# Kernel tuning notes

Hardware: AMD Instinct MI355X
Metric: run time of the kernel (lower is better)

## Reference

```python
import jax, jax.numpy as jnp
import numpy as np

KD, KY, KX = 3, 3, 3  # kernel_size from init_kwargs


def setup_inputs() -> dict:
    key = jax.random.key(0)
    x = jax.random.normal(key, (4, 2, 64, 256, 256), dtype=jnp.float32)
    return {"x": x}


def reference(x):
    # x: [B, CH, D, H, W]
    B, CH, D, H, W = x.shape
    pd, py, px = (KD - 1) // 2, (KY - 1) // 2, (KX - 1) // 2
    # replicate padding (torch F.pad mode='replicate' == jnp.pad mode='edge')
    xp = jnp.pad(x, ((0, 0), (0, 0), (pd, pd), (py, py), (px, px)), mode='edge')
    center = (KD * KY * KX) // 2  # flattened center position, excluded from max
    # running max over the 26 non-center neighbors; never materializes the
    # [B, CH, 27, D, H, W] tensor the torch conv3d path creates.
    max_nc = jnp.full(x.shape, -jnp.inf, dtype=x.dtype)
    idx = 0
    for i in range(KD):
        for j in range(KY):
            for k in range(KX):
                if idx != center:
                    shifted = xp[:, :, i:i + D, j:j + H, k:k + W]
                    max_nc = jnp.maximum(max_nc, shifted)
                idx += 1
    mask = x > max_nc  # strict local maximum (excluding self)
    return x * mask.astype(x.dtype)
```

## Files before the change

kernel.cpp:

```cpp
#include <hip/hip_runtime.h>


constexpr int D_   = 64;
constexpr int H_   = 256;
constexpr int W_   = 256;
constexpr int HW_  = H_ * W_;
constexpr int NVOL = 8;
constexpr int DC   = 8;

__device__ __forceinline__ float f3(float a, float b, float c) {
    return fmaxf(fmaxf(a, b), c);
}

__global__ __launch_bounds__(256, 4)
void nms3d(const float* __restrict__ x, float* __restrict__ out)
{
    const int tx = threadIdx.x;
    const int ty = threadIdx.y;
    const int h  = (blockIdx.y << 2) + ty;
    const int n  = blockIdx.z;
    const int z0 = blockIdx.x * DC;

    const float* __restrict__ base  = x   + (size_t)n * D_ * HW_;
    float* __restrict__       obase = out + (size_t)n * D_ * HW_;

    const int r0 = (h == 0)      ? 0      : h - 1;
    const int r2 = (h == H_ - 1) ? H_ - 1 : h + 1;
    const int c  = tx << 2;

    const float* spA = base + (size_t)max(z0 - 1, 0) * HW_;
    const float* spB = base + (size_t)z0 * HW_;
    float4 a0 = *(const float4*)(spA + r0 * W_ + c);
    float4 b0 = *(const float4*)(spA + h  * W_ + c);
    float4 d0 = *(const float4*)(spA + r2 * W_ + c);
    float4 a1 = *(const float4*)(spB + r0 * W_ + c);
    float4 b1 = *(const float4*)(spB + h  * W_ + c);
    float4 d1 = *(const float4*)(spB + r2 * W_ + c);

    float4 vm9_pp = {0,0,0,0};
    float4 vm9_p  = {0,0,0,0};
    float4 cr8_p  = {0,0,0,0};
    float4 vprev  = {0,0,0,0};

#pragma unroll
    for (int t = 0; t < DC + 2; ++t) {
        const int zi = z0 - 1 + t;

        const int zn = min(zi + 2, D_ - 1);
        const float* spn = base + (size_t)zn * HW_;
        const float4 a2 = *(const float4*)(spn + r0 * W_ + c);
        const float4 b2 = *(const float4*)(spn + h  * W_ + c);
        const float4 d2 = *(const float4*)(spn + r2 * W_ + c);

        float4 va;
        va.x = fmaxf(a0.x, d0.x); va.y = fmaxf(a0.y, d0.y);
        va.z = fmaxf(a0.z, d0.z); va.w = fmaxf(a0.w, d0.w);

        float vaL = __shfl_up(va.w, 1);   if (tx == 0)  vaL = va.x;
        float vaR = __shfl_down(va.x, 1); if (tx == 63) vaR = va.w;
        float bL  = __shfl_up(b0.w, 1);   if (tx == 0)  bL  = b0.x;
        float bR  = __shfl_down(b0.x, 1); if (tx == 63) bR  = b0.w;

        float4 hv;
        hv.x = f3(vaL, va.x, va.y);  hv.y = f3(va.x, va.y, va.z);
        hv.z = f3(va.y, va.z, va.w); hv.w = f3(va.z, va.w, vaR);
        float4 nb;
        nb.x = fmaxf(bL, b0.y);  nb.y = fmaxf(b0.x, b0.z);
        nb.z = fmaxf(b0.y, b0.w); nb.w = fmaxf(b0.z, bR);

        float4 c8, cur;
        c8.x  = fmaxf(hv.x, nb.x); c8.y  = fmaxf(hv.y, nb.y);
        c8.z  = fmaxf(hv.z, nb.z); c8.w  = fmaxf(hv.w, nb.w);
        cur.x = fmaxf(c8.x, b0.x); cur.y = fmaxf(c8.y, b0.y);
        cur.z = fmaxf(c8.z, b0.z); cur.w = fmaxf(c8.w, b0.w);

        if (zi > z0) {
            float4 mx, o;
            mx.x = f3(vm9_pp.x, cr8_p.x, cur.x);
            mx.y = f3(vm9_pp.y, cr8_p.y, cur.y);
            mx.z = f3(vm9_pp.z, cr8_p.z, cur.z);
            mx.w = f3(vm9_pp.w, cr8_p.w, cur.w);
            o.x = vprev.x > mx.x ? vprev.x : 0.0f;
            o.y = vprev.y > mx.y ? vprev.y : 0.0f;
            o.z = vprev.z > mx.z ? vprev.z : 0.0f;
            o.w = vprev.w > mx.w ? vprev.w : 0.0f;
            *(float4*)(obase + (size_t)(zi - 1) * HW_ + (size_t)h * W_ + c) = o;
        }
        vm9_pp = vm9_p; vm9_p = cur; cr8_p = c8; vprev = b0;
        a0 = a1; b0 = b1; d0 = d1;
        a1 = a2; b1 = b2; d1 = d2;
    }
}

extern "C" void kernel_launch(void* const* d_in, const int* in_sizes, int n_in,
                              void* d_out, int out_size, void* d_ws, size_t ws_size,
                              hipStream_t stream)
{
    const float* x = (const float*)d_in[0];
    float* out = (float*)d_out;
    dim3 block(64, 4, 1);
    dim3 grid(D_ / DC, H_ / 4, NVOL);
    nms3d<<<grid, block, 0, stream>>>(x, out);
}
```

Measured before the change: 230.2 us.

## Stage depth slices through LDS with async global_load_lds triple buffering

```diff
diff --git a/kernel.cpp b/kernel.cpp
--- a/kernel.cpp
+++ b/kernel.cpp
@@ -7,35 +7,52 @@
 constexpr int HW_  = H_ * W_;
 constexpr int NVOL = 8;
 constexpr int DC   = 8;
+constexpr int RY   = 8;
+constexpr int RS   = RY + 2;
+constexpr int NBUF = 3;
+constexpr int S    = DC + 2;
 
 __device__ __forceinline__ float f3(float a, float b, float c) {
     return fmaxf(fmaxf(a, b), c);
 }
 
-__global__ __launch_bounds__(256, 4)
+__device__ __forceinline__ void gload16(const float* g, float* l) {
+    __builtin_amdgcn_global_load_lds(
+        (const __attribute__((address_space(1))) void*)g,
+        (__attribute__((address_space(3))) void*)l,
+        16, 0, 0);
+}
+
+__global__ __launch_bounds__(512, 6)
 void nms3d(const float* __restrict__ x, float* __restrict__ out)
 {
+    __shared__ float lds[NBUF][RS * W_];
+
     const int tx = threadIdx.x;
     const int ty = threadIdx.y;
-    const int h  = (blockIdx.y << 2) + ty;
+    const int h0 = blockIdx.y * RY;
+    const int h  = h0 + ty;
     const int n  = blockIdx.z;
     const int z0 = blockIdx.x * DC;
+    const int c  = tx << 2;
 
     const float* __restrict__ base  = x   + (size_t)n * D_ * HW_;
     float* __restrict__       obase = out + (size_t)n * D_ * HW_;
 
-    const int r0 = (h == 0)      ? 0      : h - 1;
-    const int r2 = (h == H_ - 1) ? H_ - 1 : h + 1;
-    const int c  = tx << 2;
+    const int grA = min(max(h0 - 1 + ty, 0), H_ - 1);
+    const int grB = min(max(h0 - 1 + RY + ty, 0), H_ - 1);
+    const float* gA = base + (size_t)grA * W_ + c;
+    const float* gB = base + (size_t)grB * W_ + c;
 
-    const float* spA = base + (size_t)max(z0 - 1, 0) * HW_;
-    const float* spB = base + (size_t)z0 * HW_;
-    float4 a0 = *(const float4*)(spA + r0 * W_ + c);
-    float4 b0 = *(const float4*)(spA + h  * W_ + c);
-    float4 d0 = *(const float4*)(spA + r2 * W_ + c);
-    float4 a1 = *(const float4*)(spB + r0 * W_ + c);
-    float4 b1 = *(const float4*)(spB + h  * W_ + c);
-    float4 d1 = *(const float4*)(spB + r2 * W_ + c);
+    auto stage = [&](int t) {
+        const int zc = min(max(z0 - 1 + t, 0), D_ - 1);
+        const size_t zo = (size_t)zc * HW_;
+        float* lp = &lds[t % NBUF][0];
+        gload16(gA + zo, lp + ty * W_);
+        if (ty < 2) gload16(gB + zo, lp + (RY + ty) * W_);
+    };
+
+    stage(0);
 
     float4 vm9_pp = {0,0,0,0};
     float4 vm9_p  = {0,0,0,0};
@@ -43,14 +60,21 @@
     float4 vprev  = {0,0,0,0};
 
 #pragma unroll
-    for (int t = 0; t < DC + 2; ++t) {
-        const int zi = z0 - 1 + t;
+    for (int t = 0; t < S; ++t) {
+        if (t + 1 < S) {
+            stage(t + 1);
+            if (ty < 2) asm volatile("s_waitcnt vmcnt(2)" ::: "memory");
+            else        asm volatile("s_waitcnt vmcnt(1)" ::: "memory");
+        } else {
+            asm volatile("s_waitcnt vmcnt(0)" ::: "memory");
+        }
+        __builtin_amdgcn_s_barrier();
+        asm volatile("" ::: "memory");
 
-        const int zn = min(zi + 2, D_ - 1);
-        const float* spn = base + (size_t)zn * HW_;
-        const float4 a2 = *(const float4*)(spn + r0 * W_ + c);
-        const float4 b2 = *(const float4*)(spn + h  * W_ + c);
-        const float4 d2 = *(const float4*)(spn + r2 * W_ + c);
+        const float* p = &lds[t % NBUF][0];
+        const float4 a0 = *(const float4*)(p + (ty    ) * W_ + c);
+        const float4 b0 = *(const float4*)(p + (ty + 1) * W_ + c);
+        const float4 d0 = *(const float4*)(p + (ty + 2) * W_ + c);
 
         float4 va;
         va.x = fmaxf(a0.x, d0.x); va.y = fmaxf(a0.y, d0.y);
@@ -61,11 +85,10 @@
         float bL  = __shfl_up(b0.w, 1);   if (tx == 0)  bL  = b0.x;
         float bR  = __shfl_down(b0.x, 1); if (tx == 63) bR  = b0.w;
 
-        float4 hv;
+        float4 hv, nb;
         hv.x = f3(vaL, va.x, va.y);  hv.y = f3(va.x, va.y, va.z);
         hv.z = f3(va.y, va.z, va.w); hv.w = f3(va.z, va.w, vaR);
-        float4 nb;
-        nb.x = fmaxf(bL, b0.y);  nb.y = fmaxf(b0.x, b0.z);
+        nb.x = fmaxf(bL,  b0.y);  nb.y = fmaxf(b0.x, b0.z);
         nb.z = fmaxf(b0.y, b0.w); nb.w = fmaxf(b0.z, bR);
 
         float4 c8, cur;
@@ -74,7 +97,8 @@
         cur.x = fmaxf(c8.x, b0.x); cur.y = fmaxf(c8.y, b0.y);
         cur.z = fmaxf(c8.z, b0.z); cur.w = fmaxf(c8.w, b0.w);
 
-        if (zi > z0) {
+        if (t >= 2) {
+            const int zi = z0 - 1 + t;
             float4 mx, o;
             mx.x = f3(vm9_pp.x, cr8_p.x, cur.x);
             mx.y = f3(vm9_pp.y, cr8_p.y, cur.y);
@@ -87,8 +111,6 @@
             *(float4*)(obase + (size_t)(zi - 1) * HW_ + (size_t)h * W_ + c) = o;
         }
         vm9_pp = vm9_p; vm9_p = cur; cr8_p = c8; vprev = b0;
-        a0 = a1; b0 = b1; d0 = d1;
-        a1 = a2; b1 = b2; d1 = d2;
     }
 }
 
@@ -98,7 +120,7 @@
 {
     const float* x = (const float*)d_in[0];
     float* out = (float*)d_out;
-    dim3 block(64, 4, 1);
-    dim3 grid(D_ / DC, H_ / 4, NVOL);
+    dim3 block(64, RY, 1);
+    dim3 grid(D_ / DC, H_ / RY, NVOL);
     nms3d<<<grid, block, 0, stream>>>(x, out);
 }
```

New measurement: 233.4 us. About the same (+1.4%).

## Process four rows per thread with a rotating three-slice register window and prefetch

Applied to the files above, without the earlier changes.

```diff
diff --git a/kernel.cpp b/kernel.cpp
--- a/kernel.cpp
+++ b/kernel.cpp
@@ -1,95 +1,119 @@
 #include <hip/hip_runtime.h>
 
 
-constexpr int D_   = 64;
-constexpr int H_   = 256;
-constexpr int W_   = 256;
-constexpr int HW_  = H_ * W_;
-constexpr int NVOL = 8;
-constexpr int DC   = 8;
+constexpr int D_  = 64;
+constexpr int H_  = 256;
+constexpr int W_  = 256;
+constexpr int HW_ = H_ * W_;
+constexpr int DC  = 11;
+constexpr int S   = DC + 2;
+constexpr int PF  = 3;
 
 __device__ __forceinline__ float f3(float a, float b, float c) {
     return fmaxf(fmaxf(a, b), c);
 }
 
-__global__ __launch_bounds__(256, 4)
+__global__ __launch_bounds__(256, 3)
 void nms3d(const float* __restrict__ x, float* __restrict__ out)
 {
-    const int tx = threadIdx.x;
-    const int ty = threadIdx.y;
-    const int h  = (blockIdx.y << 2) + ty;
-    const int n  = blockIdx.z;
-    const int z0 = blockIdx.x * DC;
+    const int tx  = threadIdx.x;
+    const int ty  = threadIdx.y;
+    const int bid = blockIdx.x;
+    const int n    = bid & 7;
+    const int rest = bid >> 3;
+    const int rg   = rest & 15;
+    const int ck   = rest >> 4;
+    const int z0   = ck * DC;
+    const int R0   = (rg << 4) + (ty << 2);
+    const int c    = tx << 2;
 
     const float* __restrict__ base  = x   + (size_t)n * D_ * HW_;
     float* __restrict__       obase = out + (size_t)n * D_ * HW_;
 
-    const int r0 = (h == 0)      ? 0      : h - 1;
-    const int r2 = (h == H_ - 1) ? H_ - 1 : h + 1;
-    const int c  = tx << 2;
+    const int ro0 = max(R0 - 1, 0) * W_ + c;
+    const int ro1 = (R0    ) * W_ + c;
+    const int ro2 = (R0 + 1) * W_ + c;
+    const int ro3 = (R0 + 2) * W_ + c;
+    const int ro4 = (R0 + 3) * W_ + c;
+    const int ro5 = min(R0 + 4, H_ - 1) * W_ + c;
 
-    const float* spA = base + (size_t)max(z0 - 1, 0) * HW_;
-    const float* spB = base + (size_t)z0 * HW_;
-    float4 a0 = *(const float4*)(spA + r0 * W_ + c);
-    float4 b0 = *(const float4*)(spA + h  * W_ + c);
-    float4 d0 = *(const float4*)(spA + r2 * W_ + c);
-    float4 a1 = *(const float4*)(spB + r0 * W_ + c);
-    float4 b1 = *(const float4*)(spB + h  * W_ + c);
-    float4 d1 = *(const float4*)(spB + r2 * W_ + c);
+    float4 wA[6], wB[6], wC[6];
+    float4 vm9p[4], m2[4], vprev[4];
 
-    float4 vm9_pp = {0,0,0,0};
-    float4 vm9_p  = {0,0,0,0};
-    float4 cr8_p  = {0,0,0,0};
-    float4 vprev  = {0,0,0,0};
+#define LOADSET(WSET, SLICE) do {                                      \
+        const int zc_ = min(max(z0 - 1 + (SLICE), 0), D_ - 1);         \
+        const float* sp_ = base + (size_t)zc_ * HW_;                   \
+        WSET[0] = *(const float4*)(sp_ + ro0);                         \
+        WSET[1] = *(const float4*)(sp_ + ro1);                         \
+        WSET[2] = *(const float4*)(sp_ + ro2);                         \
+        WSET[3] = *(const float4*)(sp_ + ro3);                         \
+        WSET[4] = *(const float4*)(sp_ + ro4);                         \
+        WSET[5] = *(const float4*)(sp_ + ro5);                         \
+    } while (0)
+
+    LOADSET(wA, 0);
+    LOADSET(wB, 1);
+    LOADSET(wC, 2);
 
 #pragma unroll
-    for (int t = 0; t < DC + 2; ++t) {
-        const int zi = z0 - 1 + t;
+    for (int r = 0; r < 4; ++r) {
+        vm9p[r]  = make_float4(0.f, 0.f, 0.f, 0.f);
+        m2[r]    = make_float4(0.f, 0.f, 0.f, 0.f);
+        vprev[r] = make_float4(0.f, 0.f, 0.f, 0.f);
+    }
 
-        const int zn = min(zi + 2, D_ - 1);
-        const float* spn = base + (size_t)zn * HW_;
-        const float4 a2 = *(const float4*)(spn + r0 * W_ + c);
-        const float4 b2 = *(const float4*)(spn + h  * W_ + c);
-        const float4 d2 = *(const float4*)(spn + r2 * W_ + c);
+#define STEP(T, WCUR) do {                                             \
+        const int zo_ = z0 + (T) - 2;                                  \
+        _Pragma("unroll")                                              \
+        for (int r = 0; r < 4; ++r) {                                  \
+            const float4 up = WCUR[r], dn = WCUR[r + 2], b0 = WCUR[r + 1]; \
+            float4 va;                                                 \
+            va.x = fmaxf(up.x, dn.x); va.y = fmaxf(up.y, dn.y);        \
+            va.z = fmaxf(up.z, dn.z); va.w = fmaxf(up.w, dn.w);        \
+            float vaL = __shfl_up(va.w, 1);   if (tx == 0)  vaL = va.x; \
+            float vaR = __shfl_down(va.x, 1); if (tx == 63) vaR = va.w; \
+            float bL  = __shfl_up(b0.w, 1);   if (tx == 0)  bL  = b0.x; \
+            float bR  = __shfl_down(b0.x, 1); if (tx == 63) bR  = b0.w; \
+            float4 hv, nb, c8, cur;                                    \
+            hv.x = f3(vaL, va.x, va.y);  hv.y = f3(va.x, va.y, va.z);  \
+            hv.z = f3(va.y, va.z, va.w); hv.w = f3(va.z, va.w, vaR);   \
+            nb.x = fmaxf(bL,  b0.y);  nb.y = fmaxf(b0.x, b0.z);        \
+            nb.z = fmaxf(b0.y, b0.w); nb.w = fmaxf(b0.z, bR);          \
+            c8.x = fmaxf(hv.x, nb.x); c8.y = fmaxf(hv.y, nb.y);        \
+            c8.z = fmaxf(hv.z, nb.z); c8.w = fmaxf(hv.w, nb.w);        \
+            cur.x = fmaxf(c8.x, b0.x); cur.y = fmaxf(c8.y, b0.y);      \
+            cur.z = fmaxf(c8.z, b0.z); cur.w = fmaxf(c8.w, b0.w);      \
+            if ((T) >= 2 && zo_ < D_) {                                \
+                float4 mx, o;                                          \
+                mx.x = fmaxf(m2[r].x, cur.x);                          \
+                mx.y = fmaxf(m2[r].y, cur.y);                          \
+                mx.z = fmaxf(m2[r].z, cur.z);                          \
+                mx.w = fmaxf(m2[r].w, cur.w);                          \
+                o.x = vprev[r].x > mx.x ? vprev[r].x : 0.0f;           \
+                o.y = vprev[r].y > mx.y ? vprev[r].y : 0.0f;           \
+                o.z = vprev[r].z > mx.z ? vprev[r].z : 0.0f;           \
+                o.w = vprev[r].w > mx.w ? vprev[r].w : 0.0f;           \
+                *(float4*)(obase + (size_t)zo_ * HW_ +                 \
+                           (size_t)(R0 + r) * W_ + c) = o;             \
+            }                                                          \
+            float4 t2;                                                 \
+            t2.x = fmaxf(vm9p[r].x, c8.x);                             \
+            t2.y = fmaxf(vm9p[r].y, c8.y);                             \
+            t2.z = fmaxf(vm9p[r].z, c8.z);                             \
+            t2.w = fmaxf(vm9p[r].w, c8.w);                             \
+            m2[r] = t2; vm9p[r] = cur; vprev[r] = b0;                  \
+        }                                                              \
+        if ((T) + PF < S) LOADSET(WCUR, (T) + PF);                     \
+    } while (0)
 
-        float4 va;
-        va.x = fmaxf(a0.x, d0.x); va.y = fmaxf(a0.y, d0.y);
-        va.z = fmaxf(a0.z, d0.z); va.w = fmaxf(a0.w, d0.w);
+    STEP(0,  wA); STEP(1,  wB); STEP(2,  wC);
+    STEP(3,  wA); STEP(4,  wB); STEP(5,  wC);
+    STEP(6,  wA); STEP(7,  wB); STEP(8,  wC);
+    STEP(9,  wA); STEP(10, wB); STEP(11, wC);
+    STEP(12, wA);
 
-        float vaL = __shfl_up(va.w, 1);   if (tx == 0)  vaL = va.x;
-        float vaR = __shfl_down(va.x, 1); if (tx == 63) vaR = va.w;
-        float bL  = __shfl_up(b0.w, 1);   if (tx == 0)  bL  = b0.x;
-        float bR  = __shfl_down(b0.x, 1); if (tx == 63) bR  = b0.w;
-
-        float4 hv;
-        hv.x = f3(vaL, va.x, va.y);  hv.y = f3(va.x, va.y, va.z);
-        hv.z = f3(va.y, va.z, va.w); hv.w = f3(va.z, va.w, vaR);
-        float4 nb;
-        nb.x = fmaxf(bL, b0.y);  nb.y = fmaxf(b0.x, b0.z);
-        nb.z = fmaxf(b0.y, b0.w); nb.w = fmaxf(b0.z, bR);
-
-        float4 c8, cur;
-        c8.x  = fmaxf(hv.x, nb.x); c8.y  = fmaxf(hv.y, nb.y);
-        c8.z  = fmaxf(hv.z, nb.z); c8.w  = fmaxf(hv.w, nb.w);
-        cur.x = fmaxf(c8.x, b0.x); cur.y = fmaxf(c8.y, b0.y);
-        cur.z = fmaxf(c8.z, b0.z); cur.w = fmaxf(c8.w, b0.w);
-
-        if (zi > z0) {
-            float4 mx, o;
-            mx.x = f3(vm9_pp.x, cr8_p.x, cur.x);
-            mx.y = f3(vm9_pp.y, cr8_p.y, cur.y);
-            mx.z = f3(vm9_pp.z, cr8_p.z, cur.z);
-            mx.w = f3(vm9_pp.w, cr8_p.w, cur.w);
-            o.x = vprev.x > mx.x ? vprev.x : 0.0f;
-            o.y = vprev.y > mx.y ? vprev.y : 0.0f;
-            o.z = vprev.z > mx.z ? vprev.z : 0.0f;
-            o.w = vprev.w > mx.w ? vprev.w : 0.0f;
-            *(float4*)(obase + (size_t)(zi - 1) * HW_ + (size_t)h * W_ + c) = o;
-        }
-        vm9_pp = vm9_p; vm9_p = cur; cr8_p = c8; vprev = b0;
-        a0 = a1; b0 = b1; d0 = d1;
-        a1 = a2; b1 = b2; d1 = d2;
-    }
+#undef STEP
+#undef LOADSET
 }
 
 extern "C" void kernel_launch(void* const* d_in, const int* in_sizes, int n_in,
@@ -99,6 +123,6 @@
     const float* x = (const float*)d_in[0];
     float* out = (float*)d_out;
     dim3 block(64, 4, 1);
-    dim3 grid(D_ / DC, H_ / 4, NVOL);
+    dim3 grid(8 * 16 * 6, 1, 1);
     nms3d<<<grid, block, 0, stream>>>(x, out);
 }
```

Result: slower. 240.5 us (+4.5%).
